# Optimization experiments

Measured on AMD Instinct MI355X. Metric: run time of the kernel, lower is better.

## Reference

```python
import jax, jax.numpy as jnp
import numpy as np
from jax import lax

BN_EPS = 1e-5


def _conv(x, w):
    # stride-1, VALID conv; the torch 'locally connected' layer shares weights
    # across pixels, so it is exactly a standard conv2d.
    return lax.conv_general_dilated(
        x, w, window_strides=(1, 1), padding='VALID',
        dimension_numbers=('NCHW', 'OIHW', 'NCHW'))


def _batchnorm(x, gamma, beta):
    # training-mode BatchNorm2d: batch statistics over (N, H, W)
    mean = jnp.mean(x, axis=(0, 2, 3), keepdims=True)
    var = jnp.var(x, axis=(0, 2, 3), keepdims=True)
    xhat = (x - mean) * lax.rsqrt(var + BN_EPS)
    return xhat * gamma[None, :, None, None] + beta[None, :, None, None]


def setup_inputs() -> dict:
    key = jax.random.key(0)
    ks = jax.random.split(key, 6)
    B = 16384
    x = jax.random.normal(ks[0], (B, 256), dtype=jnp.float32)
    w1 = jax.random.normal(ks[1], (16, 1, 3, 3), dtype=jnp.float32)
    w2 = jax.random.normal(ks[2], (32, 16, 2, 2), dtype=jnp.float32)
    w3 = jax.random.normal(ks[3], (64, 32, 1, 1), dtype=jnp.float32)
    fan_in = 64 * 13 * 13
    bound = 1.0 / np.sqrt(fan_in)
    fc_w = jax.random.uniform(ks[4], (10, fan_in), minval=-bound, maxval=bound, dtype=jnp.float32)
    fc_b = jax.random.uniform(ks[5], (10,), minval=-bound, maxval=bound, dtype=jnp.float32)
    return {
        'x': x, 'w1': w1, 'w2': w2, 'w3': w3,
        'g1': jnp.ones((16,), jnp.float32), 'b1': jnp.zeros((16,), jnp.float32),
        'g2': jnp.ones((32,), jnp.float32), 'b2': jnp.zeros((32,), jnp.float32),
        'g3': jnp.ones((64,), jnp.float32), 'b3': jnp.zeros((64,), jnp.float32),
        'fc_w': fc_w, 'fc_b': fc_b,
    }


def reference(x, w1, w2, w3, g1, b1, g2, b2, g3, b3, fc_w, fc_b):
    h = x.reshape(-1, 1, 16, 16)                     # [B,1,16,16]
    h = jax.nn.relu(_batchnorm(_conv(h, w1), g1, b1))  # [B,16,14,14]
    h = jax.nn.relu(_batchnorm(_conv(h, w2), g2, b2))  # [B,32,13,13]
    h = jax.nn.relu(_batchnorm(_conv(h, w3), g3, b3))  # [B,64,13,13]
    h = h.reshape(h.shape[0], -1)                    # [B, 64*13*13]
    # dropout is identity in eval/deterministic mode
    return h @ fc_w.T + fc_b                         # [B,10]
```

## Files before the change

### kernel.cpp

```cpp
#include <hip/hip_runtime.h>


#define NPART 1024
#define P2_OFF 32768
#define ST_OFF 229376
#define ST1 ST_OFF
#define ST2 (ST_OFF + 32)
#define ST3 (ST_OFF + 96)
#define C2R_OFF 230400
#define C1R_OFF 231424
#define C2P_OFF 262144
#define A2G_BYTE 5242880ull
#define FCB_N (13 * 8192)
#define A1S 24
#define A1B 384
#define A3P 1048

typedef __attribute__((ext_vector_type(8))) short bf16x8;
typedef __attribute__((ext_vector_type(4))) float f32x4;

__device__ __forceinline__ unsigned int f2bf(float f) {
  unsigned int u = __float_as_uint(f);
  return (u + 0x7fffu + ((u >> 16) & 1u)) >> 16;
}
__device__ __forceinline__ unsigned int pkbf(float a, float b) {
  unsigned ua = __float_as_uint(a) + 0x8000u;
  unsigned ub = __float_as_uint(b) + 0x8000u;
  return __builtin_amdgcn_perm(ub, ua, 0x07060302u);
}
__device__ __forceinline__ short cvtbf(float a) {
  return (short)((__float_as_uint(a) + 0x8000u) >> 16);
}

__device__ __forceinline__ void conv1_mfma(
    const float* __restrict__ sxi,
    short* ph_buf,
    int r, int b, int q, bf16x8 a1f, f32x4 c1i)
{
  bf16x8 bf = {0, 0, 0, 0, 0, 0, 0, 0};
  unsigned* bu = (unsigned*)&bf;
  if (q == 0) {
    bu[0] = pkbf(sxi[r * 16 + b],           sxi[r * 16 + b + 1]);
    bu[1] = pkbf(sxi[r * 16 + b + 2],       sxi[(r + 1) * 16 + b]);
    bu[2] = pkbf(sxi[(r + 1) * 16 + b + 1], sxi[(r + 1) * 16 + b + 2]);
    bu[3] = pkbf(sxi[(r + 2) * 16 + b],     sxi[(r + 2) * 16 + b + 1]);
  } else if (q == 1) {
    bu[0] = pkbf(sxi[(r + 2) * 16 + b + 2], 0.f);
  }
  f32x4 acc = c1i;
  acc = __builtin_amdgcn_mfma_f32_16x16x32_bf16(a1f, bf, acc, 0, 0, 0);
  float v0 = acc[0] > 0.f ? acc[0] : 0.f;
  float v1 = acc[1] > 0.f ? acc[1] : 0.f;
  float v2 = acc[2] > 0.f ? acc[2] : 0.f;
  float v3 = acc[3] > 0.f ? acc[3] : 0.f;
  uint2 pk;
  pk.x = pkbf(v0, v1);
  pk.y = pkbf(v2, v3);
  *(uint2*)(ph_buf + (r & 1) * A1B + b * A1S + 4 * q) = pk;
}

__device__ __forceinline__ bf16x8 conv1_afrag(const float* w1, float rs1b,
                                              int b, int q) {
  bf16x8 v;
#pragma unroll
  for (int j = 0; j < 8; ++j) {
    int tap = 8 * q + j;
    v[j] = (tap < 9) ? (short)f2bf(w1[b * 9 + tap] * rs1b) : (short)0;
  }
  return v;
}

__global__ __launch_bounds__(256) void k1_xsyrk(
    const float* __restrict__ x, float* __restrict__ parts)
{
  __shared__ float sx[16 * 256];
  const int tid = threadIdx.x, w = tid >> 6, lane = tid & 63;
  const int b = lane & 15, q = lane >> 4;
  {
    const float4* xs = (const float4*)(x + (size_t)blockIdx.x * (16 * 256));
    float4* sd = (float4*)sx;
    for (int e = tid; e < 16 * 64; e += 256) sd[e] = xs[e];
  }
  __syncthreads();
  const int di = (b < 9) ? (b / 3) : 0;
  const int dj = (b < 9) ? (b - di * 3) : 0;
  const int h = q >> 1, jb = (q & 1) * 8;
  f32x4 acc = {0.f, 0.f, 0.f, 0.f};
#pragma unroll 1
  for (int t = 0; t < 4; ++t) {
    const float* sxi = sx + (w * 4 + t) * 256;
#pragma unroll 1
    for (int s = 0; s < 7; ++s) {
      bf16x8 af;
      unsigned* au = (unsigned*)&af;
      if (b < 9) {
        const float* srow = sxi + (2 * s + h + di) * 16 + dj;
#pragma unroll
        for (int cc = 0; cc < 4; ++cc) {
          float v0 = (jb + 2 * cc     < 14) ? srow[jb + 2 * cc]     : 0.f;
          float v1 = (jb + 2 * cc + 1 < 14) ? srow[jb + 2 * cc + 1] : 0.f;
          au[cc] = pkbf(v0, v1);
        }
      } else if (b == 9) {
#pragma unroll
        for (int cc = 0; cc < 4; ++cc) {
          unsigned lo = (jb + 2 * cc     < 14) ? 0x3F80u : 0u;
          unsigned hi = (jb + 2 * cc + 1 < 14) ? 0x3F800000u : 0u;
          au[cc] = lo | hi;
        }
      } else {
#pragma unroll
        for (int cc = 0; cc < 4; ++cc) au[cc] = 0u;
      }
      acc = __builtin_amdgcn_mfma_f32_16x16x32_bf16(af, af, acc, 0, 0, 0);
    }
  }
  __syncthreads();
  float* redc = sx;
#pragma unroll
  for (int rr = 0; rr < 4; ++rr)
    redc[w * 256 + (4 * q + rr) * 16 + b] = acc[rr];
  __syncthreads();
  parts[blockIdx.x * 256 + tid] =
      redc[tid] + redc[256 + tid] + redc[512 + tid] + redc[768 + tid];
}

__global__ __launch_bounds__(256) void k_stats1a(
    const float* __restrict__ parts, float* __restrict__ ws)
{
  const int e = blockIdx.x, tid = threadIdx.x;
  const int w = tid >> 6, lane = tid & 63;
  __shared__ float rs[4];
  float s = 0.f;
#pragma unroll 4
  for (int i = tid; i < 1024; i += 256) s += parts[i * 256 + e];
#pragma unroll
  for (int d = 1; d < 64; d <<= 1) s += __shfl_xor(s, d);
  if (lane == 0) rs[w] = s;
  __syncthreads();
  if (tid == 0) ws[C1R_OFF + e] = rs[0] + rs[1] + rs[2] + rs[3];
}

__global__ __launch_bounds__(64) void k_stats1b(
    const float* __restrict__ w1, const float* __restrict__ gamma,
    const float* __restrict__ beta, float* __restrict__ ws)
{
  const int c = threadIdx.x;
  if (c >= 16) return;
  const float* C = ws + C1R_OFF;
  float wr[9];
#pragma unroll
  for (int p = 0; p < 9; ++p) wr[p] = w1[c * 9 + p];
  float msum = 0.f;
#pragma unroll
  for (int p = 0; p < 9; ++p) msum += wr[p] * C[9 * 16 + p];
  float e2 = 0.f;
#pragma unroll
  for (int a = 0; a < 9; ++a)
#pragma unroll
    for (int bb = 0; bb < 9; ++bb)
      e2 += wr[a] * wr[bb] * C[a * 16 + bb];
  const float inv_n = 1.0f / (16384.0f * 196.0f);
  float mean = msum * inv_n;
  float var  = e2 * inv_n - mean * mean;
  float sv   = gamma[c] * rsqrtf(var + 1e-5f);
  ws[ST1 + c]      = sv;
  ws[ST1 + 16 + c] = beta[c] - mean * sv;
}

__global__ __launch_bounds__(256) void k_stats2(
    const float* __restrict__ gamma, const float* __restrict__ beta,
    float* __restrict__ ws, int nch, int part_off, int st_off, float inv_n)
{
  const int c = blockIdx.x, tid = threadIdx.x;
  const int w = tid >> 6, lane = tid & 63;
  __shared__ float rs[4], rq[4];
  float s = 0.f, q = 0.f;
#pragma unroll 4
  for (int i = tid; i < NPART; i += 256) {
    s += ws[part_off + i * 2 * nch + c];
    q += ws[part_off + i * 2 * nch + nch + c];
  }
#pragma unroll
  for (int d = 1; d < 64; d <<= 1) {
    s += __shfl_xor(s, d);
    q += __shfl_xor(q, d);
  }
  if (lane == 0) { rs[w] = s; rq[w] = q; }
  __syncthreads();
  if (tid == 0) {
    float st = rs[0] + rs[1] + rs[2] + rs[3];
    float qt = rq[0] + rq[1] + rq[2] + rq[3];
    float mean = st * inv_n;
    float var  = qt * inv_n - mean * mean;
    float sv   = gamma[c] * rsqrtf(var + 1e-5f);
    ws[st_off + c]       = sv;
    ws[st_off + nch + c] = beta[c] - mean * sv;
  }
}

__global__ __launch_bounds__(256) void k3_conv2_stats(
    const float* __restrict__ x, const float* __restrict__ w1,
    const float* __restrict__ w2, float* __restrict__ ws)
{
  __shared__ float sx_s[16 * 256 + 16];
  __shared__ alignas(16) short a1h[4 * 2 * A1B];
  __shared__ float redf[256];
  const int tid = threadIdx.x, w = tid >> 6, lane = tid & 63;
  const int b = lane & 15, q = lane >> 4;
  {
    const float4* xs = (const float4*)(x + (size_t)blockIdx.x * (16 * 256));
    float4* sd = (float4*)sx_s;
    for (int e = tid; e < 16 * 64; e += 256) sd[e] = xs[e];
    if (tid < 16) sx_s[16 * 256 + tid] = 0.f;
  }
  bf16x8 a1f = conv1_afrag(w1, ws[ST1 + b], b, q);
  f32x4 c1i;
#pragma unroll
  for (int r = 0; r < 4; ++r) c1i[r] = ws[ST1 + 16 + 4 * q + r];
  bf16x8 b2h[4];
#pragma unroll
  for (int ks = 0; ks < 2; ++ks)
#pragma unroll
    for (int nt = 0; nt < 2; ++nt) {
      bf16x8 vh;
#pragma unroll
      for (int j = 0; j < 8; ++j) {
        int kk = 8 * (q & 1) + j, dj = q >> 1;
        vh[j] = (short)f2bf(w2[(nt * 16 + b) * 64 + kk * 4 + ks * 2 + dj]);
      }
      b2h[ks * 2 + nt] = vh;
    }
  const float vb = (b < 13) ? 1.f : 0.f;
  const int colAr = (b + (q >> 1) < 15) ? (b + (q >> 1)) : 15;
  const int offAl = colAr * A1S + 8 * (q & 1);
  __syncthreads();

  float s2r[2][4] = {{0.f,0.f,0.f,0.f},{0.f,0.f,0.f,0.f}};
  float q2r[2][4] = {{0.f,0.f,0.f,0.f},{0.f,0.f,0.f,0.f}};
  short* ph = a1h + w * (2 * A1B);
#pragma unroll 1
  for (int t = 0; t < 4; ++t) {
    const float* sxi = sx_s + (w * 4 + t) * 256;
    conv1_mfma(sxi, ph, 0, b, q, a1f, c1i);
    __builtin_amdgcn_wave_barrier();
#pragma unroll 1
    for (int i = 0; i < 13; ++i) {
      conv1_mfma(sxi, ph, i + 1, b, q, a1f, c1i);
      __builtin_amdgcn_wave_barrier();
      bf16x8 ah0 = *(const bf16x8*)(ph + (i & 1) * A1B + offAl);
      bf16x8 ah1 = *(const bf16x8*)(ph + ((i + 1) & 1) * A1B + offAl);
      f32x4 acc2[2] = {{0.f,0.f,0.f,0.f},{0.f,0.f,0.f,0.f}};
#pragma unroll
      for (int nt = 0; nt < 2; ++nt) {
        acc2[nt] = __builtin_amdgcn_mfma_f32_16x16x32_bf16(b2h[nt], ah0, acc2[nt], 0, 0, 0);
        acc2[nt] = __builtin_amdgcn_mfma_f32_16x16x32_bf16(b2h[2 + nt], ah1, acc2[nt], 0, 0, 0);
      }
#pragma unroll
      for (int nt = 0; nt < 2; ++nt)
#pragma unroll
        for (int r = 0; r < 4; ++r) {
          float ym = acc2[nt][r] * vb;
          s2r[nt][r] += ym;
          q2r[nt][r] = fmaf(ym, acc2[nt][r], q2r[nt][r]);
        }
      __builtin_amdgcn_wave_barrier();
    }
  }
#pragma unroll
  for (int nt = 0; nt < 2; ++nt)
#pragma unroll
    for (int r = 0; r < 4; ++r) {
      float sv = s2r[nt][r], qv = q2r[nt][r];
      sv += __shfl_xor(sv, 1); sv += __shfl_xor(sv, 2);
      sv += __shfl_xor(sv, 4); sv += __shfl_xor(sv, 8);
      qv += __shfl_xor(qv, 1); qv += __shfl_xor(qv, 2);
      qv += __shfl_xor(qv, 4); qv += __shfl_xor(qv, 8);
      if (b == 0) {
        redf[w * 64 + nt * 16 + 4 * q + r]      = sv;
        redf[w * 64 + 32 + nt * 16 + 4 * q + r] = qv;
      }
    }
  __syncthreads();
  if (tid < 64)
    ws[P2_OFF + blockIdx.x * 64 + tid] =
        redf[tid] + redf[64 + tid] + redf[128 + tid] + redf[192 + tid];
}

__global__ __launch_bounds__(256) void k5_a2(
    const float* __restrict__ x, const float* __restrict__ w1,
    const float* __restrict__ w2, float* __restrict__ ws,
    short* __restrict__ a2g, float* __restrict__ parts)
{
  __shared__ float sx_s[16 * 256 + 16];
  __shared__ alignas(16) short a1h[4 * 2 * A1B];
  __shared__ alignas(16) short xt4[4 * 32 * 40];
  __shared__ float s2red[4 * 32];
  const int tid = threadIdx.x, w = tid >> 6, lane = tid & 63;
  const int b = lane & 15, q = lane >> 4;
  {
    const float4* xs = (const float4*)(x + (size_t)blockIdx.x * (16 * 256));
    float4* sd = (float4*)sx_s;
    for (int e = tid; e < 16 * 64; e += 256) sd[e] = xs[e];
    if (tid < 16) sx_s[16 * 256 + tid] = 0.f;
  }
  bf16x8 a1f = conv1_afrag(w1, ws[ST1 + b], b, q);
  f32x4 c1i;
#pragma unroll
  for (int r = 0; r < 4; ++r) c1i[r] = ws[ST1 + 16 + 4 * q + r];
  bf16x8 b2h[4];
#pragma unroll
  for (int ks = 0; ks < 2; ++ks)
#pragma unroll
    for (int nt = 0; nt < 2; ++nt) {
      float rs2b = ws[ST2 + nt * 16 + b];
      bf16x8 vh;
#pragma unroll
      for (int j = 0; j < 8; ++j) {
        int kk = 8 * (q & 1) + j, dj = q >> 1;
        vh[j] = (short)f2bf(w2[(nt * 16 + b) * 64 + kk * 4 + ks * 2 + dj] * rs2b);
      }
      b2h[ks * 2 + nt] = vh;
    }
  f32x4 c2i[2];
#pragma unroll
  for (int nt = 0; nt < 2; ++nt)
#pragma unroll
    for (int r = 0; r < 4; ++r)
      c2i[nt][r] = (b < 13) ? ws[ST2 + 32 + nt * 16 + 4 * q + r] : -1e30f;
  const int colAr = (b + (q >> 1) < 15) ? (b + (q >> 1)) : 15;
  const int offAl = colAr * A1S + 8 * (q & 1);
  short* xt = xt4 + w * 1280;
  __syncthreads();

  f32x4 accT0 = {0.f,0.f,0.f,0.f}, accT1 = {0.f,0.f,0.f,0.f},
        accT2 = {0.f,0.f,0.f,0.f};
  float s2aR[2][4] = {{0.f,0.f,0.f,0.f},{0.f,0.f,0.f,0.f}};
  short* ph = a1h + w * (2 * A1B);
#pragma unroll 1
  for (int t = 0; t < 4; ++t) {
    const int img = blockIdx.x * 16 + w * 4 + t;
    const float* sxi = sx_s + (w * 4 + t) * 256;
    conv1_mfma(sxi, ph, 0, b, q, a1f, c1i);
    __builtin_amdgcn_wave_barrier();
#pragma unroll 1
    for (int i = 0; i < 13; ++i) {
      conv1_mfma(sxi, ph, i + 1, b, q, a1f, c1i);
      __builtin_amdgcn_wave_barrier();
      bf16x8 ah0 = *(const bf16x8*)(ph + (i & 1) * A1B + offAl);
      bf16x8 ah1 = *(const bf16x8*)(ph + ((i + 1) & 1) * A1B + offAl);
#pragma unroll
      for (int nt = 0; nt < 2; ++nt) {
        f32x4 acc2 = c2i[nt];
        acc2 = __builtin_amdgcn_mfma_f32_16x16x32_bf16(b2h[nt], ah0, acc2, 0, 0, 0);
        acc2 = __builtin_amdgcn_mfma_f32_16x16x32_bf16(b2h[2 + nt], ah1, acc2, 0, 0, 0);
        float vm[4];
#pragma unroll
        for (int r = 0; r < 4; ++r) {
          vm[r] = acc2[r] > 0.f ? acc2[r] : 0.f;
          s2aR[nt][r] += vm[r];
          xt[(nt * 16 + 4 * q + r) * 40 + (i & 1) * 16 + b] = cvtbf(vm[r]);
        }
        if (b < 13) {
          uint2 pk;
          pk.x = pkbf(vm[0], vm[1]);
          pk.y = pkbf(vm[2], vm[3]);
          *(uint2*)(a2g + (size_t)img * 5408 + (size_t)(i * 13 + b) * 32 +
                    nt * 16 + 4 * q) = pk;
        }
      }
      __builtin_amdgcn_wave_barrier();
      if (i & 1) {
        bf16x8 xf0 = *(const bf16x8*)(xt + b * 40 + 8 * q);
        bf16x8 xf1 = *(const bf16x8*)(xt + (16 + b) * 40 + 8 * q);
        accT0 = __builtin_amdgcn_mfma_f32_16x16x32_bf16(xf0, xf0, accT0, 0, 0, 0);
        accT1 = __builtin_amdgcn_mfma_f32_16x16x32_bf16(xf0, xf1, accT1, 0, 0, 0);
        accT2 = __builtin_amdgcn_mfma_f32_16x16x32_bf16(xf1, xf1, accT2, 0, 0, 0);
      }
      __builtin_amdgcn_wave_barrier();
    }
    {
      uint2 z; z.x = 0u; z.y = 0u;
      *(uint2*)(xt + b * 40 + 16 + 4 * q) = z;
      *(uint2*)(xt + (16 + b) * 40 + 16 + 4 * q) = z;
      __builtin_amdgcn_wave_barrier();
      bf16x8 xf0 = *(const bf16x8*)(xt + b * 40 + 8 * q);
      bf16x8 xf1 = *(const bf16x8*)(xt + (16 + b) * 40 + 8 * q);
      accT0 = __builtin_amdgcn_mfma_f32_16x16x32_bf16(xf0, xf0, accT0, 0, 0, 0);
      accT1 = __builtin_amdgcn_mfma_f32_16x16x32_bf16(xf0, xf1, accT1, 0, 0, 0);
      accT2 = __builtin_amdgcn_mfma_f32_16x16x32_bf16(xf1, xf1, accT2, 0, 0, 0);
      __builtin_amdgcn_wave_barrier();
    }
  }
#pragma unroll
  for (int nt = 0; nt < 2; ++nt)
#pragma unroll
    for (int r = 0; r < 4; ++r) {
      float sv = s2aR[nt][r];
      sv += __shfl_xor(sv, 1); sv += __shfl_xor(sv, 2);
      sv += __shfl_xor(sv, 4); sv += __shfl_xor(sv, 8);
      if (b == 0) s2red[w * 32 + nt * 16 + 4 * q + r] = sv;
    }
  float* redc = sx_s;
#pragma unroll
  for (int rr = 0; rr < 4; ++rr) {
    int m = 4 * q + rr;
    redc[w * 1024 + 0   + m * 16 + b] = accT0[rr];
    redc[w * 1024 + 256 + m * 16 + b] = accT1[rr];
    redc[w * 1024 + 512 + m * 16 + b] = accT2[rr];
  }
  __syncthreads();
  for (int e = tid; e < 768; e += 256)
    parts[blockIdx.x * 800 + e] =
        redc[e] + redc[1024 + e] + redc[2048 + e] + redc[3072 + e];
  if (tid < 32)
    parts[blockIdx.x * 800 + 768 + tid] =
        s2red[tid] + s2red[32 + tid] + s2red[64 + tid] + s2red[96 + tid];
}

__global__ __launch_bounds__(256) void k_statsC(
    const float* __restrict__ parts, float* __restrict__ ws)
{
  const int e = blockIdx.x, tid = threadIdx.x;
  const int w = tid >> 6, lane = tid & 63;
  __shared__ float rs[4];
  float s = 0.f;
#pragma unroll 4
  for (int i = tid; i < 1024; i += 256) s += parts[i * 800 + e];
#pragma unroll
  for (int d = 1; d < 64; d <<= 1) s += __shfl_xor(s, d);
  if (lane == 0) rs[w] = s;
  __syncthreads();
  if (tid == 0) ws[C2R_OFF + e] = rs[0] + rs[1] + rs[2] + rs[3];
}

__global__ __launch_bounds__(64) void k_stats3n(
    const float* __restrict__ w3, const float* __restrict__ gamma,
    const float* __restrict__ beta, float* __restrict__ ws)
{
  const int c3 = threadIdx.x;
  if (c3 >= 64) return;
  const float* C2R = ws + C2R_OFF;
  float wr[32];
#pragma unroll
  for (int k = 0; k < 32; ++k) wr[k] = w3[c3 * 32 + k];
  const float inv_n = 1.0f / (16384.0f * 169.0f);
  float msum = 0.f;
#pragma unroll
  for (int k = 0; k < 32; ++k) msum += wr[k] * C2R[768 + k];
  float e2 = 0.f;
  for (int a = 0; a < 16; ++a)
#pragma unroll
    for (int bb = 0; bb < 16; ++bb) {
      e2 += wr[a] * wr[bb] * C2R[a * 16 + bb];
      e2 += wr[16 + a] * wr[16 + bb] * C2R[512 + a * 16 + bb];
      e2 += 2.f * wr[a] * wr[16 + bb] * C2R[256 + a * 16 + bb];
    }
  float mean = msum * inv_n;
  float var  = e2 * inv_n - mean * mean;
  float sv   = gamma[c3] * rsqrtf(var + 1e-5f);
  ws[ST3 + c3]      = sv;
  ws[ST3 + 64 + c3] = beta[c3] - mean * sv;
}

__global__ __launch_bounds__(256) void k0_fcB(
    const float* __restrict__ fcw, unsigned int* __restrict__ fcB)
{
  int F = blockIdx.x * 256 + threadIdx.x;
  if (F >= FCB_N) return;
  int u = F & 3, q = (F >> 2) & 3, jj = (F >> 4) & 15;
  int mm = (F >> 8) & 31, i = F >> 13;
  int k0 = mm * 32 + q * 8 + u * 2;
  unsigned lo = 0, hi = 0;
  if (jj < 10) {
    int c0 = k0 >> 4, j0 = k0 & 15;
    if (j0 < 13) lo = f2bf(fcw[jj * 10816 + c0 * 169 + i * 13 + j0]);
    int c1 = (k0 + 1) >> 4, j1 = (k0 + 1) & 15;
    if (j1 < 13) hi = f2bf(fcw[jj * 10816 + c1 * 169 + i * 13 + j1]);
  }
  fcB[F] = lo | (hi << 16);
}

__global__ __launch_bounds__(256) void k7_fc(
    const short* __restrict__ a2g, const float* __restrict__ w3,
    const float* __restrict__ fcb, const float* __restrict__ ws,
    float* __restrict__ out)
{
  __shared__ alignas(16) short a3buf[16 * A3P];
  const int tid = threadIdx.x, w = tid >> 6, lane = tid & 63;
  const int b = lane & 15, q = lane >> 4;
  bf16x8 b3h[4];
  f32x4 c3i[4];
#pragma unroll
  for (int nt = 0; nt < 4; ++nt) {
    float s3 = ws[ST3 + nt * 16 + b];
    float t3 = ws[ST3 + 64 + nt * 16 + b];
    bf16x8 vh;
#pragma unroll
    for (int j = 0; j < 8; ++j)
      vh[j] = (short)f2bf(w3[(nt * 16 + b) * 32 + 8 * q + j] * s3);
    b3h[nt] = vh;
    c3i[nt][0] = t3;
#pragma unroll
    for (int r = 1; r < 4; ++r)
      c3i[nt][r] = (q < 3) ? t3 : -1e30f;
  }
  const bf16x8* fcB = (const bf16x8*)ws;
  f32x4 accF = {0.f, 0.f, 0.f, 0.f};
  const int pixc = (b < 12) ? b : 12;
  size_t ib[4];
#pragma unroll
  for (int t = 0; t < 4; ++t)
    ib[t] = (size_t)(blockIdx.x * 16 + w * 4 + t) * 5408;
  bf16x8 a2pre[4];
#pragma unroll
  for (int t = 0; t < 4; ++t)
    a2pre[t] = *(const bf16x8*)(a2g + ib[t] + pixc * 32 + 8 * q);

#pragma unroll 1
  for (int i = 0; i < 13; ++i) {
    bf16x8 a2cur[4];
#pragma unroll
    for (int t = 0; t < 4; ++t) a2cur[t] = a2pre[t];
    if (i < 12) {
#pragma unroll
      for (int t = 0; t < 4; ++t)
        a2pre[t] = *(const bf16x8*)(a2g + ib[t] +
                                    (size_t)((i + 1) * 13 + pixc) * 32 + 8 * q);
    }
#pragma unroll
    for (int t = 0; t < 4; ++t) {
      const int g = w * 4 + t;
#pragma unroll
      for (int nt = 0; nt < 4; ++nt) {
        f32x4 acc3 = c3i[nt];
        acc3 = __builtin_amdgcn_mfma_f32_16x16x32_bf16(a2cur[t], b3h[nt], acc3, 0, 0, 0);
        float v0 = acc3[0] > 0.f ? acc3[0] : 0.f;
        float v1 = acc3[1] > 0.f ? acc3[1] : 0.f;
        float v2 = acc3[2] > 0.f ? acc3[2] : 0.f;
        float v3 = acc3[3] > 0.f ? acc3[3] : 0.f;
        uint2 pk2;
        pk2.x = pkbf(v0, v1);
        pk2.y = pkbf(v2, v3);
        *(uint2*)(a3buf + g * A3P + (nt * 16 + b) * 16 + 4 * q) = pk2;
      }
    }
    __syncthreads();
#pragma unroll
    for (int mm = 0; mm < 8; ++mm) {
      bf16x8 af = *(const bf16x8*)(a3buf + b * A3P + w * 256 + mm * 32 + 8 * q);
      bf16x8 bw = fcB[((i * 32 + w * 8 + mm) * 16 + b) * 4 + q];
      accF = __builtin_amdgcn_mfma_f32_16x16x32_bf16(af, bw, accF, 0, 0, 0);
    }
    __syncthreads();
  }

  float* redf7 = (float*)a3buf;
#pragma unroll
  for (int r = 0; r < 4; ++r)
    redf7[w * 256 + (4 * q + r) * 16 + b] = accF[r];
  __syncthreads();
  if (tid < 160) {
    int img = tid / 10, jj = tid - img * 10;
    float s = redf7[img * 16 + jj] + redf7[256 + img * 16 + jj] +
              redf7[512 + img * 16 + jj] + redf7[768 + img * 16 + jj];
    out[(blockIdx.x * 16 + img) * 10 + jj] = s + fcb[jj];
  }
}

extern "C" void kernel_launch(void* const* d_in, const int* in_sizes, int n_in,
                              void* d_out, int out_size, void* d_ws, size_t ws_size,
                              hipStream_t stream) {
  (void)in_sizes; (void)n_in; (void)out_size; (void)ws_size;
  const float* x   = (const float*)d_in[0];
  const float* w1  = (const float*)d_in[1];
  const float* w2  = (const float*)d_in[2];
  const float* w3  = (const float*)d_in[3];
  const float* g1  = (const float*)d_in[4];
  const float* b1  = (const float*)d_in[5];
  const float* g2  = (const float*)d_in[6];
  const float* b2  = (const float*)d_in[7];
  const float* g3  = (const float*)d_in[8];
  const float* b3  = (const float*)d_in[9];
  const float* fcw = (const float*)d_in[10];
  const float* fcb = (const float*)d_in[11];
  float* out = (float*)d_out;
  float* ws  = (float*)d_ws;
  short* a2g = (short*)((char*)d_ws + A2G_BYTE);
  float* parts = ws + C2P_OFF;

  k1_xsyrk<<<1024, 256, 0, stream>>>(x, parts);
  k_stats1a<<<256, 256, 0, stream>>>(parts, ws);
  k_stats1b<<<1, 64, 0, stream>>>(w1, g1, b1, ws);
  k3_conv2_stats<<<1024, 256, 0, stream>>>(x, w1, w2, ws);
  k_stats2<<<32, 256, 0, stream>>>(g2, b2, ws, 32, P2_OFF, ST2,
                                   1.0f / (16384.0f * 169.0f));
  k5_a2<<<1024, 256, 0, stream>>>(x, w1, w2, ws, a2g, parts);
  k_statsC<<<800, 256, 0, stream>>>(parts, ws);
  k_stats3n<<<1, 64, 0, stream>>>(w3, g3, b3, ws);
  k0_fcB<<<FCB_N / 256, 256, 0, stream>>>(fcw, (unsigned int*)ws);
  k7_fc<<<1024, 256, 0, stream>>>(a2g, w3, fcb, ws, out);
}
```

Before: 280.6 us.

## Swap conv2 MFMA operands to keep Gram fragments in registers, sum via MFMA

Swaps the A/B operands of the conv2 MFMA so each lane holds outputs for one channel across four pixel columns. Consecutive rows' packed bf16 results can then be combined in registers to form the Gram-matrix fragments, which removes the per-wave LDS transpose buffer and its barriers. Per-channel sums are computed with MFMAs against a vector of ones instead of shuffle reductions. In exchange, the global a2g stores become scattered 16-bit writes rather than packed 8-byte stores. Channel sums are also now taken from bf16-rounded values, which may shift the statistics slightly.

Result: no change. 279.5 us (-0.4%).

```diff
diff --git a/kernel.cpp b/kernel.cpp
--- a/kernel.cpp
+++ b/kernel.cpp
@@ -18,6 +18,7 @@
 
 typedef __attribute__((ext_vector_type(8))) short bf16x8;
 typedef __attribute__((ext_vector_type(4))) float f32x4;
+typedef __attribute__((ext_vector_type(4))) unsigned int u32x4;
 
 __device__ __forceinline__ unsigned int f2bf(float f) {
   unsigned int u = __float_as_uint(f);
@@ -30,6 +31,10 @@
 }
 __device__ __forceinline__ short cvtbf(float a) {
   return (short)((__float_as_uint(a) + 0x8000u) >> 16);
+}
+__device__ __forceinline__ bf16x8 mkfrag(uint2 a, uint2 b) {
+  u32x4 u = {a.x, a.y, b.x, b.y};
+  return __builtin_bit_cast(bf16x8, u);
 }
 
 __device__ __forceinline__ void conv1_mfma(
@@ -294,7 +299,6 @@
 {
   __shared__ float sx_s[16 * 256 + 16];
   __shared__ alignas(16) short a1h[4 * 2 * A1B];
-  __shared__ alignas(16) short xt4[4 * 32 * 40];
   __shared__ float s2red[4 * 32];
   const int tid = threadIdx.x, w = tid >> 6, lane = tid & 63;
   const int b = lane & 15, q = lane >> 4;
@@ -324,83 +328,88 @@
     }
   f32x4 c2i[2];
 #pragma unroll
-  for (int nt = 0; nt < 2; ++nt)
+  for (int nt = 0; nt < 2; ++nt) {
+    float t2b = ws[ST2 + 32 + nt * 16 + b];
 #pragma unroll
     for (int r = 0; r < 4; ++r)
-      c2i[nt][r] = (b < 13) ? ws[ST2 + 32 + nt * 16 + 4 * q + r] : -1e30f;
+      c2i[nt][r] = (4 * q + r < 13) ? t2b : -1e30f;
+  }
   const int colAr = (b + (q >> 1) < 15) ? (b + (q >> 1)) : 15;
   const int offAl = colAr * A1S + 8 * (q & 1);
-  short* xt = xt4 + w * 1280;
+  const u32x4 ou = {0x3F803F80u, 0x3F803F80u, 0x3F803F80u, 0x3F803F80u};
+  const bf16x8 ones = __builtin_bit_cast(bf16x8, ou);
   __syncthreads();
 
   f32x4 accT0 = {0.f,0.f,0.f,0.f}, accT1 = {0.f,0.f,0.f,0.f},
         accT2 = {0.f,0.f,0.f,0.f};
-  float s2aR[2][4] = {{0.f,0.f,0.f,0.f},{0.f,0.f,0.f,0.f}};
+  f32x4 accS0 = {0.f,0.f,0.f,0.f}, accS1 = {0.f,0.f,0.f,0.f};
   short* ph = a1h + w * (2 * A1B);
 #pragma unroll 1
   for (int t = 0; t < 4; ++t) {
     const int img = blockIdx.x * 16 + w * 4 + t;
     const float* sxi = sx_s + (w * 4 + t) * 256;
+    short* p0 = a2g + (size_t)img * 5408 + (size_t)(4 * q) * 32 + b;
     conv1_mfma(sxi, ph, 0, b, q, a1f, c1i);
     __builtin_amdgcn_wave_barrier();
+    uint2 pkp[2];
 #pragma unroll 1
     for (int i = 0; i < 13; ++i) {
       conv1_mfma(sxi, ph, i + 1, b, q, a1f, c1i);
       __builtin_amdgcn_wave_barrier();
       bf16x8 ah0 = *(const bf16x8*)(ph + (i & 1) * A1B + offAl);
       bf16x8 ah1 = *(const bf16x8*)(ph + ((i + 1) & 1) * A1B + offAl);
+      uint2 pkc[2];
 #pragma unroll
       for (int nt = 0; nt < 2; ++nt) {
         f32x4 acc2 = c2i[nt];
-        acc2 = __builtin_amdgcn_mfma_f32_16x16x32_bf16(b2h[nt], ah0, acc2, 0, 0, 0);
-        acc2 = __builtin_amdgcn_mfma_f32_16x16x32_bf16(b2h[2 + nt], ah1, acc2, 0, 0, 0);
-        float vm[4];
-#pragma unroll
-        for (int r = 0; r < 4; ++r) {
-          vm[r] = acc2[r] > 0.f ? acc2[r] : 0.f;
-          s2aR[nt][r] += vm[r];
-          xt[(nt * 16 + 4 * q + r) * 40 + (i & 1) * 16 + b] = cvtbf(vm[r]);
+        acc2 = __builtin_amdgcn_mfma_f32_16x16x32_bf16(ah0, b2h[nt], acc2, 0, 0, 0);
+        acc2 = __builtin_amdgcn_mfma_f32_16x16x32_bf16(ah1, b2h[2 + nt], acc2, 0, 0, 0);
+        float v0 = acc2[0] > 0.f ? acc2[0] : 0.f;
+        float v1 = acc2[1] > 0.f ? acc2[1] : 0.f;
+        float v2 = acc2[2] > 0.f ? acc2[2] : 0.f;
+        float v3 = acc2[3] > 0.f ? acc2[3] : 0.f;
+        uint2 pk;
+        pk.x = pkbf(v0, v1);
+        pk.y = pkbf(v2, v3);
+        short* pp = p0 + nt * 16;
+        pp[0] = (short)pk.x;
+        if (q < 3) {
+          pp[32] = (short)(pk.x >> 16);
+          pp[64] = (short)pk.y;
+          pp[96] = (short)(pk.y >> 16);
         }
-        if (b < 13) {
-          uint2 pk;
-          pk.x = pkbf(vm[0], vm[1]);
-          pk.y = pkbf(vm[2], vm[3]);
-          *(uint2*)(a2g + (size_t)img * 5408 + (size_t)(i * 13 + b) * 32 +
-                    nt * 16 + 4 * q) = pk;
-        }
-      }
-      __builtin_amdgcn_wave_barrier();
+        pkc[nt] = pk;
+      }
+      p0 += 416;
       if (i & 1) {
-        bf16x8 xf0 = *(const bf16x8*)(xt + b * 40 + 8 * q);
-        bf16x8 xf1 = *(const bf16x8*)(xt + (16 + b) * 40 + 8 * q);
+        bf16x8 xf0 = mkfrag(pkp[0], pkc[0]);
+        bf16x8 xf1 = mkfrag(pkp[1], pkc[1]);
         accT0 = __builtin_amdgcn_mfma_f32_16x16x32_bf16(xf0, xf0, accT0, 0, 0, 0);
         accT1 = __builtin_amdgcn_mfma_f32_16x16x32_bf16(xf0, xf1, accT1, 0, 0, 0);
         accT2 = __builtin_amdgcn_mfma_f32_16x16x32_bf16(xf1, xf1, accT2, 0, 0, 0);
+        accS0 = __builtin_amdgcn_mfma_f32_16x16x32_bf16(ones, xf0, accS0, 0, 0, 0);
+        accS1 = __builtin_amdgcn_mfma_f32_16x16x32_bf16(ones, xf1, accS1, 0, 0, 0);
+      } else {
+        pkp[0] = pkc[0];
+        pkp[1] = pkc[1];
       }
       __builtin_amdgcn_wave_barrier();
     }
     {
-      uint2 z; z.x = 0u; z.y = 0u;
-      *(uint2*)(xt + b * 40 + 16 + 4 * q) = z;
-      *(uint2*)(xt + (16 + b) * 40 + 16 + 4 * q) = z;
-      __builtin_amdgcn_wave_barrier();
-      bf16x8 xf0 = *(const bf16x8*)(xt + b * 40 + 8 * q);
-      bf16x8 xf1 = *(const bf16x8*)(xt + (16 + b) * 40 + 8 * q);
+      uint2 zz; zz.x = 0u; zz.y = 0u;
+      bf16x8 xf0 = mkfrag(pkp[0], zz);
+      bf16x8 xf1 = mkfrag(pkp[1], zz);
       accT0 = __builtin_amdgcn_mfma_f32_16x16x32_bf16(xf0, xf0, accT0, 0, 0, 0);
       accT1 = __builtin_amdgcn_mfma_f32_16x16x32_bf16(xf0, xf1, accT1, 0, 0, 0);
       accT2 = __builtin_amdgcn_mfma_f32_16x16x32_bf16(xf1, xf1, accT2, 0, 0, 0);
-      __builtin_amdgcn_wave_barrier();
-    }
-  }
-#pragma unroll
-  for (int nt = 0; nt < 2; ++nt)
-#pragma unroll
-    for (int r = 0; r < 4; ++r) {
-      float sv = s2aR[nt][r];
-      sv += __shfl_xor(sv, 1); sv += __shfl_xor(sv, 2);
-      sv += __shfl_xor(sv, 4); sv += __shfl_xor(sv, 8);
-      if (b == 0) s2red[w * 32 + nt * 16 + 4 * q + r] = sv;
-    }
+      accS0 = __builtin_amdgcn_mfma_f32_16x16x32_bf16(ones, xf0, accS0, 0, 0, 0);
+      accS1 = __builtin_amdgcn_mfma_f32_16x16x32_bf16(ones, xf1, accS1, 0, 0, 0);
+    }
+  }
+  if (q == 0) {
+    s2red[w * 32 + b]      = accS0[0];
+    s2red[w * 32 + 16 + b] = accS1[0];
+  }
   float* redc = sx_s;
 #pragma unroll
   for (int rr = 0; rr < 4; ++rr) {
```
